# Kernel tuning notes

Hardware: AMD Instinct MI355X
Metric: run time of the kernel (lower is better)

The kernel has to match this reference:

```python
import jax, jax.numpy as jnp
import numpy as np

BN_EPS = 1e-5

def _square_distance(src, dst):
    # src: (B,N,3), dst: (B,S,3) -> (B,N,S)
    d = -2.0 * jnp.einsum('bnc,bsc->bns', src, dst)
    d = d + jnp.sum(src * src, -1)[:, :, None]
    d = d + jnp.sum(dst * dst, -1)[:, None, :]
    return d

def _bn_relu(x, gamma, beta):
    # x: (B,N,C); training-mode batchnorm over (B,N)
    mean = jnp.mean(x, axis=(0, 1))
    var = jnp.mean(jnp.square(x - mean), axis=(0, 1))
    y = (x - mean) * jax.lax.rsqrt(var + BN_EPS) * gamma + beta
    return jax.nn.relu(y)

def setup_inputs() -> dict:
    key = jax.random.key(0)
    ks = jax.random.split(key, 12)
    B, N, S, D1, D2 = 8, 8192, 2048, 128, 256
    in_ch, mlp = 384, [256, 256]
    inp = {
        'xyz1': jax.random.normal(ks[0], (B, 3, N), jnp.float32),
        'xyz2': jax.random.normal(ks[1], (B, 3, S), jnp.float32),
        'points1': jax.random.normal(ks[2], (B, D1, N), jnp.float32),
        'points2': jax.random.normal(ks[3], (B, D2, S), jnp.float32),
    }
    last = in_ch
    for i, out in enumerate(mlp):
        inp[f'W{i+1}'] = jax.random.normal(ks[4 + 2 * i], (out, last), jnp.float32) * (1.0 / np.sqrt(last))
        inp[f'b{i+1}'] = jnp.zeros((out,), jnp.float32)
        inp[f'g{i+1}'] = jnp.ones((out,), jnp.float32)
        inp[f'beta{i+1}'] = jnp.zeros((out,), jnp.float32)
        last = out
    return inp

def reference(xyz1, xyz2, points1, points2, W1, b1, g1, beta1, W2, b2, g2, beta2):
    p1 = jnp.transpose(xyz1, (0, 2, 1))   # (B,N,3)
    p2 = jnp.transpose(xyz2, (0, 2, 1))   # (B,S,3)
    f2 = jnp.transpose(points2, (0, 2, 1))  # (B,S,D2)

    dists = _square_distance(p1, p2)      # (B,N,S)
    neg_d, idx = jax.lax.top_k(-dists, 3)  # 3 smallest distances
    d3 = -neg_d                            # (B,N,3)
    dist_recip = 1.0 / (d3 + 1e-8)
    weight = dist_recip / jnp.sum(dist_recip, axis=2, keepdims=True)  # (B,N,3)

    gathered = jax.vmap(lambda p, i: p[i])(f2, idx)   # (B,N,3,D2)
    interp = jnp.sum(gathered * weight[..., None], axis=2)  # (B,N,D2)

    f1 = jnp.transpose(points1, (0, 2, 1))  # (B,N,D1)
    x = jnp.concatenate([f1, interp], axis=-1)  # (B,N,D1+D2)

    x = _bn_relu(jnp.einsum('bnc,oc->bno', x, W1) + b1, g1, beta1)
    x = _bn_relu(jnp.einsum('bnc,oc->bno', x, W2) + b2, g2, beta2)
    return jnp.transpose(x, (0, 2, 1))  # (B,256,N)
```

## Files before the change

kernel.cpp:

```cpp
#include <hip/hip_runtime.h>

#define B_   8
#define N_   8192
#define S_   2048
#define D1_  128
#define D2_  256
#define O_   256
#define BN_  (B_*N_)

typedef __bf16 bf16;
typedef __bf16 bf16x8_t __attribute__((ext_vector_type(8)));
typedef __bf16 bf16x4_t __attribute__((ext_vector_type(4)));
typedef float  f32x4_t  __attribute__((ext_vector_type(4)));

static const size_t OFF_IDX  = 0;
static const size_t OFF_W    = 786432;
static const size_t OFF_XP   = 1572864;
static const size_t OFF_Z    = 51904512;
static const size_t OFF_SS1  = 85458944;
static const size_t OFF_SS2  = 85460992;
static const size_t OFF_PART = 85463040;

__global__ __launch_bounds__(256) void k_conv_p1(const float* __restrict__ p1, bf16* __restrict__ xp) {
  const int g  = blockIdx.x * 256 + threadIdx.x;
  const int n4 = g & 2047;
  const int c8 = (g >> 11) & 15;
  const int b  = g >> 15;
  const int n  = n4 * 4;
  const float* src = p1 + ((size_t)b * D1_ + c8 * 8) * N_ + n;
  bf16x8_t o0, o1, o2, o3;
  #pragma unroll
  for (int j = 0; j < 8; ++j) {
    float4 v = *(const float4*)(src + (size_t)j * N_);
    o0[j] = (bf16)v.x; o1[j] = (bf16)v.y; o2[j] = (bf16)v.z; o3[j] = (bf16)v.w;
  }
  bf16* dst = xp + (((size_t)b * 48 + c8) * N_ + n) * 8;
  *(bf16x8_t*)(dst)      = o0;
  *(bf16x8_t*)(dst + 8)  = o1;
  *(bf16x8_t*)(dst + 16) = o2;
  *(bf16x8_t*)(dst + 24) = o3;
}

__device__ __forceinline__ void ins3(float d, int i,
                                     float& d0, float& d1, float& d2,
                                     int& i0, int& i1, int& i2) {
  const bool c2 = d < d2, c1 = d < d1, c0 = d < d0;
  const float nd2 = c1 ? d1 : (c2 ? d : d2); const int ni2 = c1 ? i1 : (c2 ? i : i2);
  const float nd1 = c0 ? d0 : (c1 ? d : d1); const int ni1 = c0 ? i0 : (c1 ? i : i1);
  d0 = c0 ? d : d0; i0 = c0 ? i : i0;
  d1 = nd1; i1 = ni1; d2 = nd2; i2 = ni2;
}

__global__ __launch_bounds__(256) void k_nn3(const float* __restrict__ xyz1, const float* __restrict__ xyz2,
                                             int* __restrict__ idxw, float* __restrict__ www) {
  __shared__ float4 sq[4][S_ / 4];
  __shared__ float  pd[4][64][3];
  __shared__ int    pi[4][64][3];
  const int tid  = threadIdx.x;
  const int lane = tid & 63, w = tid >> 6;
  const int b     = blockIdx.y;
  const int nbase = blockIdx.x * 64;

  const float* x2 = xyz2 + (size_t)b * 3 * S_;
  for (int j = tid; j < S_ / 4; j += 256) {
    const float4 x = *(const float4*)(x2 + 4 * j);
    const float4 y = *(const float4*)(x2 + S_ + 4 * j);
    const float4 z = *(const float4*)(x2 + 2 * S_ + 4 * j);
    float4 qq;
    qq.x = fmaf(x.x, x.x, fmaf(y.x, y.x, z.x * z.x));
    qq.y = fmaf(x.y, x.y, fmaf(y.y, y.y, z.y * z.y));
    qq.z = fmaf(x.z, x.z, fmaf(y.z, y.z, z.z * z.z));
    qq.w = fmaf(x.w, x.w, fmaf(y.w, y.w, z.w * z.w));
    sq[0][j] = x; sq[1][j] = y; sq[2][j] = z; sq[3][j] = qq;
  }

  const int n = nbase + lane;
  const float* x1 = xyz1 + (size_t)b * 3 * N_;
  const float px = x1[n], py = x1[N_ + n], pz = x1[2 * N_ + n];
  const float ax = -2.f * px, ay = -2.f * py, az = -2.f * pz;
  __syncthreads();

  float e0 = 3.4e38f, e1 = 3.4e38f, e2 = 3.4e38f;
  int   i0 = 0, i1 = 0, i2 = 0;

  const int jb = w * (S_ / 16);
  #pragma unroll 4
  for (int j = jb; j < jb + S_ / 16; ++j) {
    const float4 qx = sq[0][j], qy = sq[1][j], qz = sq[2][j], qq = sq[3][j];
    #define CAND(C, SI)                                                        \
      {                                                                        \
        const float E = fmaf(ax, qx.C, fmaf(ay, qy.C, fmaf(az, qz.C, qq.C))); \
        const bool l0 = E < e0, l1 = E < e1, l2 = E < e2;                      \
        const int ni1 = l0 ? i0 : (l1 ? (SI) : i1);                            \
        const int ni2 = l1 ? i1 : (l2 ? (SI) : i2);                            \
        i0 = l0 ? (SI) : i0; i1 = ni1; i2 = ni2;                               \
        const float ne1 = __builtin_amdgcn_fmed3f(E, e0, e1);                  \
        const float ne2 = __builtin_amdgcn_fmed3f(E, e1, e2);                  \
        e0 = fminf(E, e0); e1 = ne1; e2 = ne2;                                 \
      }
    CAND(x, 4 * j + 0)
    CAND(y, 4 * j + 1)
    CAND(z, 4 * j + 2)
    CAND(w, 4 * j + 3)
    #undef CAND
  }

  const float pp = fmaf(px, px, fmaf(py, py, pz * pz));
  pd[w][lane][0] = e0 + pp; pd[w][lane][1] = e1 + pp; pd[w][lane][2] = e2 + pp;
  pi[w][lane][0] = i0; pi[w][lane][1] = i1; pi[w][lane][2] = i2;
  __syncthreads();

  if (tid < 64) {
    float d0 = pd[0][tid][0], d1 = pd[0][tid][1], d2 = pd[0][tid][2];
    int   j0 = pi[0][tid][0], j1 = pi[0][tid][1], j2 = pi[0][tid][2];
    #pragma unroll
    for (int ck = 1; ck < 4; ++ck)
      #pragma unroll
      for (int k = 0; k < 3; ++k)
        ins3(pd[ck][tid][k], pi[ck][tid][k], d0, d1, d2, j0, j1, j2);
    const float r0 = 1.f / (d0 + 1e-8f), r1 = 1.f / (d1 + 1e-8f), r2 = 1.f / (d2 + 1e-8f);
    const float inv = 1.f / (r0 + r1 + r2);
    const int bn = b * N_ + nbase + tid;
    idxw[bn] = j0; idxw[BN_ + bn] = j1; idxw[2 * BN_ + bn] = j2;
    www[bn] = r0 * inv; www[BN_ + bn] = r1 * inv; www[2 * BN_ + bn] = r2 * inv;
  }
}

__global__ __launch_bounds__(256) void k_t2(const float* __restrict__ p2, bf16* __restrict__ f2t) {
  __shared__ float lds[64][65];
  const int bid = blockIdx.x;
  const int b = bid & 7;
  const int inner = bid >> 3;
  const int s0 = (inner & 31) * 64;
  const int c0 = (inner >> 5) * 64;
  const int t = threadIdx.x;
  {
    const int cr = t >> 2, scb = (t & 3) * 16;
    const float* src = p2 + ((size_t)b * D2_ + c0 + cr) * S_ + s0 + scb;
    #pragma unroll
    for (int i = 0; i < 4; ++i) {
      const float4 v = *(const float4*)(src + 4 * i);
      lds[cr][scb + 4 * i + 0] = v.x; lds[cr][scb + 4 * i + 1] = v.y;
      lds[cr][scb + 4 * i + 2] = v.z; lds[cr][scb + 4 * i + 3] = v.w;
    }
  }
  __syncthreads();
  const int co = (t & 7) * 8;
  #pragma unroll
  for (int pass = 0; pass < 2; ++pass) {
    const int s = pass * 32 + (t >> 3);
    bf16x8_t o;
    #pragma unroll
    for (int j = 0; j < 8; ++j) o[j] = (bf16)lds[co + j][s];
    *(bf16x8_t*)(f2t + ((size_t)b * S_ + s0 + s) * D2_ + c0 + co) = o;
  }
}

__global__ __launch_bounds__(256) void k_interp(const bf16* __restrict__ f2t, const int* __restrict__ idxw,
                                                const float* __restrict__ www, bf16* __restrict__ xp) {
  const int bid = blockIdx.x;
  const int b = bid & 7;
  const int n = (bid >> 3) * 8 + (threadIdx.x & 7);
  const int c8 = threadIdx.x >> 3;
  const int bn = b * N_ + n;
  const int j0 = idxw[bn], j1 = idxw[BN_ + bn], j2 = idxw[2 * BN_ + bn];
  const float w0 = www[bn], w1 = www[BN_ + bn], w2 = www[2 * BN_ + bn];
  const bf16* base = f2t + (size_t)b * S_ * D2_ + c8 * 8;
  const bf16x8_t v0 = *(const bf16x8_t*)(base + (size_t)j0 * D2_);
  const bf16x8_t v1 = *(const bf16x8_t*)(base + (size_t)j1 * D2_);
  const bf16x8_t v2 = *(const bf16x8_t*)(base + (size_t)j2 * D2_);
  bf16x8_t out;
  #pragma unroll
  for (int j = 0; j < 8; ++j)
    out[j] = (bf16)(w0 * (float)v0[j] + w1 * (float)v1[j] + w2 * (float)v2[j]);
  *(bf16x8_t*)(xp + (((size_t)b * 48 + 16 + c8) * N_ + (size_t)n) * 8) = out;
}

template<int K>
__global__ __launch_bounds__(256) void k_gemm(const float* __restrict__ W, const float* __restrict__ bias,
                                              const bf16* __restrict__ X, bf16* __restrict__ Zp) {
  __shared__ bf16 As[128][40];
  __shared__ bf16 Bt[128][40];
  const int tid = threadIdx.x;
  const int lane = tid & 63, wid = tid >> 6;
  const int wr = wid >> 1, wc = wid & 1;
  const int n0 = blockIdx.x * 128;
  const int m0 = blockIdx.y * 128;
  const int b  = blockIdx.z;
  const int l15 = lane & 15, l4 = lane >> 4;

  f32x4_t acc[4][4];
  #pragma unroll
  for (int i = 0; i < 4; ++i)
    #pragma unroll
    for (int j = 0; j < 4; ++j) { f32x4_t z = {0.f, 0.f, 0.f, 0.f}; acc[i][j] = z; }

  const int arow = tid >> 1, ac0 = (tid & 1) * 16;
  const bf16* Xb = X + (size_t)b * (K / 8) * ((size_t)N_ * 8);

  for (int kt = 0; kt < K; kt += 32) {
    {
      const float* s = W + (size_t)(m0 + arow) * K + kt + ac0;
      const float4 f0 = *(const float4*)(s);
      const float4 f1 = *(const float4*)(s + 4);
      const float4 f2 = *(const float4*)(s + 8);
      const float4 f3 = *(const float4*)(s + 12);
      bf16x8_t h0, h1;
      h0[0] = (bf16)f0.x; h0[1] = (bf16)f0.y; h0[2] = (bf16)f0.z; h0[3] = (bf16)f0.w;
      h0[4] = (bf16)f1.x; h0[5] = (bf16)f1.y; h0[6] = (bf16)f1.z; h0[7] = (bf16)f1.w;
      h1[0] = (bf16)f2.x; h1[1] = (bf16)f2.y; h1[2] = (bf16)f2.z; h1[3] = (bf16)f2.w;
      h1[4] = (bf16)f3.x; h1[5] = (bf16)f3.y; h1[6] = (bf16)f3.z; h1[7] = (bf16)f3.w;
      *(bf16x8_t*)&As[arow][ac0]     = h0;
      *(bf16x8_t*)&As[arow][ac0 + 8] = h1;
    }
    {
      const bf16* s = Xb + ((size_t)(kt / 8 + wid)) * ((size_t)N_ * 8) + (size_t)n0 * 8;
      const bf16x8_t q0 = *(const bf16x8_t*)(s + (size_t)lane * 8);
      const bf16x8_t q1 = *(const bf16x8_t*)(s + (size_t)(lane + 64) * 8);
      *(bf16x8_t*)&Bt[lane][wid * 8]      = q0;
      *(bf16x8_t*)&Bt[lane + 64][wid * 8] = q1;
    }
    __syncthreads();
    bf16x8_t af[4], bfr[4];
    #pragma unroll
    for (int mi = 0; mi < 4; ++mi) af[mi]  = *(const bf16x8_t*)&As[wr * 64 + mi * 16 + l15][l4 * 8];
    #pragma unroll
    for (int ni = 0; ni < 4; ++ni) bfr[ni] = *(const bf16x8_t*)&Bt[wc * 64 + ni * 16 + l15][l4 * 8];
    #pragma unroll
    for (int mi = 0; mi < 4; ++mi)
      #pragma unroll
      for (int ni = 0; ni < 4; ++ni)
        acc[mi][ni] = __builtin_amdgcn_mfma_f32_16x16x32_bf16(af[mi], bfr[ni], acc[mi][ni], 0, 0, 0);
    __syncthreads();
  }
  bf16* Zb = Zp + (size_t)b * 32 * ((size_t)N_ * 8);
  #pragma unroll
  for (int mi = 0; mi < 4; ++mi) {
    const int obase = m0 + wr * 64 + mi * 16 + l4 * 4;
    const float4 bv = *(const float4*)(bias + obase);
    const size_t gofs = (size_t)(obase >> 3) * ((size_t)N_ * 8) + (obase & 7);
    #pragma unroll
    for (int ni = 0; ni < 4; ++ni) {
      const int nn = n0 + wc * 64 + ni * 16 + l15;
      bf16x4_t o;
      o[0] = (bf16)(acc[mi][ni][0] + bv.x);
      o[1] = (bf16)(acc[mi][ni][1] + bv.y);
      o[2] = (bf16)(acc[mi][ni][2] + bv.z);
      o[3] = (bf16)(acc[mi][ni][3] + bv.w);
      *(bf16x4_t*)(Zb + gofs + (size_t)nn * 8) = o;
    }
  }
}

__global__ __launch_bounds__(256) void k_stats_p(const bf16* __restrict__ Z, float* __restrict__ part) {
  const int og = blockIdx.x & 31, b = blockIdx.x >> 5;
  const bf16* src = Z + ((size_t)b * 32 + og) * ((size_t)N_ * 8);
  float s[8], q[8];
  #pragma unroll
  for (int j = 0; j < 8; ++j) { s[j] = 0.f; q[j] = 0.f; }
  for (int n = threadIdx.x; n < N_; n += 256) {
    const bf16x8_t v = *(const bf16x8_t*)(src + (size_t)n * 8);
    #pragma unroll
    for (int j = 0; j < 8; ++j) {
      const float f = (float)v[j];
      s[j] += f; q[j] = fmaf(f, f, q[j]);
    }
  }
  #pragma unroll
  for (int off = 1; off < 64; off <<= 1) {
    #pragma unroll
    for (int j = 0; j < 8; ++j) {
      s[j] += __shfl_xor(s[j], off);
      q[j] += __shfl_xor(q[j], off);
    }
  }
  __shared__ float red[4][16];
  const int w = threadIdx.x >> 6;
  if ((threadIdx.x & 63) == 0) {
    #pragma unroll
    for (int j = 0; j < 8; ++j) { red[w][j] = s[j]; red[w][8 + j] = q[j]; }
  }
  __syncthreads();
  if (threadIdx.x < 16) {
    const float t = red[0][threadIdx.x] + red[1][threadIdx.x] + red[2][threadIdx.x] + red[3][threadIdx.x];
    const int sel = threadIdx.x >> 3, j = threadIdx.x & 7;
    part[((size_t)sel * 256 + og * 8 + j) * 8 + b] = t;
  }
}

__global__ __launch_bounds__(256) void k_ss(const float* __restrict__ part, const float* __restrict__ g,
                                            const float* __restrict__ be, float* __restrict__ ss) {
  const int c = threadIdx.x;
  float s = 0.f, q = 0.f;
  #pragma unroll
  for (int b = 0; b < 8; ++b) { s += part[(size_t)c * 8 + b]; q += part[(256 + (size_t)c) * 8 + b]; }
  const float mean = s * (1.f / 65536.f);
  const float var  = q * (1.f / 65536.f) - mean * mean;
  const float rstd = rsqrtf(var + 1e-5f);
  const float sc = g[c] * rstd;
  ss[c] = sc; ss[O_ + c] = be[c] - mean * sc;
}

__global__ __launch_bounds__(256) void k_apply_p(bf16* __restrict__ Z, const float* __restrict__ ss) {
  const int nc = blockIdx.x & 31, og = (blockIdx.x >> 5) & 31, b = blockIdx.x >> 10;
  const int n = nc * 256 + threadIdx.x;
  bf16* p = Z + (((size_t)b * 32 + og) * N_ + n) * 8;
  bf16x8_t v = *(bf16x8_t*)p;
  #pragma unroll
  for (int j = 0; j < 8; ++j) {
    const int c = og * 8 + j;
    v[j] = (bf16)fmaxf(fmaf((float)v[j], ss[c], ss[O_ + c]), 0.f);
  }
  *(bf16x8_t*)p = v;
}

__global__ __launch_bounds__(256) void k_final_p(const bf16* __restrict__ Z, const float* __restrict__ ss,
                                                 float* __restrict__ Y) {
  const int b  = blockIdx.x >> 7;
  const int n0 = (blockIdx.x & 127) * 64;
  const int og = threadIdx.x >> 3, ns = threadIdx.x & 7;
  const bf16* src = Z + (((size_t)b * 32 + og) * N_ + n0 + ns * 8) * 8;
  bf16x8_t v[8];
  #pragma unroll
  for (int i = 0; i < 8; ++i) v[i] = *(const bf16x8_t*)(src + i * 8);
  float sc[8], sh[8];
  #pragma unroll
  for (int j = 0; j < 8; ++j) { sc[j] = ss[og * 8 + j]; sh[j] = ss[O_ + og * 8 + j]; }
  float* dst = Y + ((size_t)b * O_ + og * 8) * N_ + n0 + ns * 8;
  #pragma unroll
  for (int j = 0; j < 8; ++j) {
    float4 a0, a1;
    a0.x = fmaxf(fmaf((float)v[0][j], sc[j], sh[j]), 0.f);
    a0.y = fmaxf(fmaf((float)v[1][j], sc[j], sh[j]), 0.f);
    a0.z = fmaxf(fmaf((float)v[2][j], sc[j], sh[j]), 0.f);
    a0.w = fmaxf(fmaf((float)v[3][j], sc[j], sh[j]), 0.f);
    a1.x = fmaxf(fmaf((float)v[4][j], sc[j], sh[j]), 0.f);
    a1.y = fmaxf(fmaf((float)v[5][j], sc[j], sh[j]), 0.f);
    a1.z = fmaxf(fmaf((float)v[6][j], sc[j], sh[j]), 0.f);
    a1.w = fmaxf(fmaf((float)v[7][j], sc[j], sh[j]), 0.f);
    *(float4*)(dst + (size_t)j * N_)     = a0;
    *(float4*)(dst + (size_t)j * N_ + 4) = a1;
  }
}

extern "C" void kernel_launch(void* const* d_in, const int* in_sizes, int n_in,
                              void* d_out, int out_size, void* d_ws, size_t ws_size,
                              hipStream_t stream) {
  const float* xyz1    = (const float*)d_in[0];
  const float* xyz2    = (const float*)d_in[1];
  const float* points1 = (const float*)d_in[2];
  const float* points2 = (const float*)d_in[3];
  const float* W1  = (const float*)d_in[4];
  const float* b1  = (const float*)d_in[5];
  const float* g1  = (const float*)d_in[6];
  const float* be1 = (const float*)d_in[7];
  const float* W2  = (const float*)d_in[8];
  const float* b2  = (const float*)d_in[9];
  const float* g2  = (const float*)d_in[10];
  const float* be2 = (const float*)d_in[11];
  float* Y = (float*)d_out;
  char*  ws = (char*)d_ws;
  int*   idxw = (int*)(ws + OFF_IDX);
  float* www  = (float*)(ws + OFF_W);
  bf16*  xp   = (bf16*)(ws + OFF_XP);
  bf16*  z1   = (bf16*)(ws + OFF_Z);
  bf16*  f2t  = (bf16*)(ws + OFF_Z);
  bf16*  z2   = (bf16*)(ws + OFF_XP);
  float* ss1  = (float*)(ws + OFF_SS1);
  float* ss2  = (float*)(ws + OFF_SS2);
  float* part = (float*)(ws + OFF_PART);

  hipLaunchKernelGGL(k_conv_p1, dim3(1024), dim3(256), 0, stream, points1, xp);
  hipLaunchKernelGGL(k_nn3, dim3(128, 8), dim3(256), 0, stream, xyz1, xyz2, idxw, www);
  hipLaunchKernelGGL(k_t2, dim3(1024), dim3(256), 0, stream, points2, f2t);
  hipLaunchKernelGGL(k_interp, dim3(8192), dim3(256), 0, stream, f2t, idxw, www, xp);
  hipLaunchKernelGGL((k_gemm<384>), dim3(64, 2, 8), dim3(256), 0, stream, W1, b1, xp, z1);
  hipLaunchKernelGGL(k_stats_p, dim3(256), dim3(256), 0, stream, z1, part);
  hipLaunchKernelGGL(k_ss, dim3(1), dim3(256), 0, stream, part, g1, be1, ss1);
  hipLaunchKernelGGL(k_apply_p, dim3(8192), dim3(256), 0, stream, z1, ss1);
  hipLaunchKernelGGL((k_gemm<256>), dim3(64, 2, 8), dim3(256), 0, stream, W2, b2, z1, z2);
  hipLaunchKernelGGL(k_stats_p, dim3(256), dim3(256), 0, stream, z2, part);
  hipLaunchKernelGGL(k_ss, dim3(1), dim3(256), 0, stream, part, g2, be2, ss2);
  hipLaunchKernelGGL(k_final_p, dim3(1024), dim3(256), 0, stream, z2, ss2, Y);
}
```

Baseline: 196.4 us.

## Pre-convert weights to bf16 tile images and load GEMM tiles via global_load_lds

Adds a small kernel that converts W1/W2 to bf16 and lays them out in per-tile, k-chunk-major images. The GEMM then fills both shared-memory tiles with direct global-to-LDS 16-byte loads instead of register round-trips and per-iteration fp32-to-bf16 conversion. It also remaps the 1D grid so blocks sharing n-tiles land on the same XCD for L2 reuse. The unpadded LDS layout may raise bank conflicts on fragment reads, and there is one extra launch. The weight images reuse the idx workspace region, which is safe only because the interpolation kernel has already consumed it.

```diff
diff --git a/kernel.cpp b/kernel.cpp
--- a/kernel.cpp
+++ b/kernel.cpp
@@ -20,6 +20,10 @@
 static const size_t OFF_SS1  = 85458944;
 static const size_t OFF_SS2  = 85460992;
 static const size_t OFF_PART = 85463040;
+
+#define GL16(gsrc, ldst) \
+  __builtin_amdgcn_global_load_lds((const __attribute__((address_space(1))) void*)(gsrc), \
+                                   (__attribute__((address_space(3))) void*)(ldst), 16, 0, 0)
 
 __global__ __launch_bounds__(256) void k_conv_p1(const float* __restrict__ p1, bf16* __restrict__ xp) {
   const int g  = blockIdx.x * 256 + threadIdx.x;
@@ -176,17 +180,48 @@
   *(bf16x8_t*)(xp + (((size_t)b * 48 + 16 + c8) * N_ + (size_t)n) * 8) = out;
 }
 
+__global__ __launch_bounds__(256) void k_wprep(const float* __restrict__ W1, const float* __restrict__ W2,
+                                               bf16* __restrict__ img) {
+  const int g = blockIdx.x * 256 + threadIdx.x;
+  if (g < 12288) {
+    const int e = g * 8;
+    const int imgblk = e >> 12, r = e & 4095;
+    const int kc = r >> 10, row = (r & 1023) >> 3;
+    const int mblk = imgblk / 12, kt32 = imgblk % 12;
+    const float* s = W1 + (size_t)(mblk * 128 + row) * 384 + kt32 * 32 + kc * 8;
+    const float4 f0 = *(const float4*)(s), f1 = *(const float4*)(s + 4);
+    bf16x8_t h;
+    h[0] = (bf16)f0.x; h[1] = (bf16)f0.y; h[2] = (bf16)f0.z; h[3] = (bf16)f0.w;
+    h[4] = (bf16)f1.x; h[5] = (bf16)f1.y; h[6] = (bf16)f1.z; h[7] = (bf16)f1.w;
+    *(bf16x8_t*)(img + e) = h;
+  } else if (g < 20480) {
+    const int e = (g - 12288) * 8;
+    const int imgblk = e >> 12, r = e & 4095;
+    const int kc = r >> 10, row = (r & 1023) >> 3;
+    const int mblk = imgblk >> 3, kt32 = imgblk & 7;
+    const float* s = W2 + (size_t)(mblk * 128 + row) * 256 + kt32 * 32 + kc * 8;
+    const float4 f0 = *(const float4*)(s), f1 = *(const float4*)(s + 4);
+    bf16x8_t h;
+    h[0] = (bf16)f0.x; h[1] = (bf16)f0.y; h[2] = (bf16)f0.z; h[3] = (bf16)f0.w;
+    h[4] = (bf16)f1.x; h[5] = (bf16)f1.y; h[6] = (bf16)f1.z; h[7] = (bf16)f1.w;
+    *(bf16x8_t*)(img + 98304 + e) = h;
+  }
+}
+
 template<int K>
-__global__ __launch_bounds__(256) void k_gemm(const float* __restrict__ W, const float* __restrict__ bias,
+__global__ __launch_bounds__(256) void k_gemm(const bf16* __restrict__ Wimg, const float* __restrict__ bias,
                                               const bf16* __restrict__ X, bf16* __restrict__ Zp) {
-  __shared__ bf16 As[128][40];
-  __shared__ bf16 Bt[128][40];
+  __shared__ bf16 As[4096];
+  __shared__ bf16 Bt[4096];
   const int tid = threadIdx.x;
   const int lane = tid & 63, wid = tid >> 6;
   const int wr = wid >> 1, wc = wid & 1;
-  const int n0 = blockIdx.x * 128;
-  const int m0 = blockIdx.y * 128;
-  const int b  = blockIdx.z;
+  const int dd = blockIdx.x;
+  const int xcd = dd & 7, pos = dd >> 3;
+  const int b = pos >> 4, q = pos & 15;
+  const int m0 = (q & 1) * 128;
+  const int n0 = (xcd * 8 + (q >> 1)) * 128;
+  const int mblk = m0 >> 7;
   const int l15 = lane & 15, l4 = lane >> 4;
 
   f32x4_t acc[4][4];
@@ -195,37 +230,21 @@
     #pragma unroll
     for (int j = 0; j < 4; ++j) { f32x4_t z = {0.f, 0.f, 0.f, 0.f}; acc[i][j] = z; }
 
-  const int arow = tid >> 1, ac0 = (tid & 1) * 16;
   const bf16* Xb = X + (size_t)b * (K / 8) * ((size_t)N_ * 8);
 
   for (int kt = 0; kt < K; kt += 32) {
-    {
-      const float* s = W + (size_t)(m0 + arow) * K + kt + ac0;
-      const float4 f0 = *(const float4*)(s);
-      const float4 f1 = *(const float4*)(s + 4);
-      const float4 f2 = *(const float4*)(s + 8);
-      const float4 f3 = *(const float4*)(s + 12);
-      bf16x8_t h0, h1;
-      h0[0] = (bf16)f0.x; h0[1] = (bf16)f0.y; h0[2] = (bf16)f0.z; h0[3] = (bf16)f0.w;
-      h0[4] = (bf16)f1.x; h0[5] = (bf16)f1.y; h0[6] = (bf16)f1.z; h0[7] = (bf16)f1.w;
-      h1[0] = (bf16)f2.x; h1[1] = (bf16)f2.y; h1[2] = (bf16)f2.z; h1[3] = (bf16)f2.w;
-      h1[4] = (bf16)f3.x; h1[5] = (bf16)f3.y; h1[6] = (bf16)f3.z; h1[7] = (bf16)f3.w;
-      *(bf16x8_t*)&As[arow][ac0]     = h0;
-      *(bf16x8_t*)&As[arow][ac0 + 8] = h1;
-    }
-    {
-      const bf16* s = Xb + ((size_t)(kt / 8 + wid)) * ((size_t)N_ * 8) + (size_t)n0 * 8;
-      const bf16x8_t q0 = *(const bf16x8_t*)(s + (size_t)lane * 8);
-      const bf16x8_t q1 = *(const bf16x8_t*)(s + (size_t)(lane + 64) * 8);
-      *(bf16x8_t*)&Bt[lane][wid * 8]      = q0;
-      *(bf16x8_t*)&Bt[lane + 64][wid * 8] = q1;
-    }
+    const bf16* asrc = Wimg + (size_t)(mblk * (K / 32) + (kt >> 5)) * 4096 + wid * 1024 + lane * 8;
+    GL16(asrc,       &As[wid * 1024]);
+    GL16(asrc + 512, &As[wid * 1024 + 512]);
+    const bf16* bsrc = Xb + ((size_t)(kt >> 3) + wid) * ((size_t)N_ * 8) + ((size_t)n0 + lane) * 8;
+    GL16(bsrc,       &Bt[wid * 1024]);
+    GL16(bsrc + 512, &Bt[wid * 1024 + 512]);
     __syncthreads();
     bf16x8_t af[4], bfr[4];
     #pragma unroll
-    for (int mi = 0; mi < 4; ++mi) af[mi]  = *(const bf16x8_t*)&As[wr * 64 + mi * 16 + l15][l4 * 8];
-    #pragma unroll
-    for (int ni = 0; ni < 4; ++ni) bfr[ni] = *(const bf16x8_t*)&Bt[wc * 64 + ni * 16 + l15][l4 * 8];
+    for (int mi = 0; mi < 4; ++mi) af[mi]  = *(const bf16x8_t*)&As[l4 * 1024 + (wr * 64 + mi * 16 + l15) * 8];
+    #pragma unroll
+    for (int ni = 0; ni < 4; ++ni) bfr[ni] = *(const bf16x8_t*)&Bt[l4 * 1024 + (wc * 64 + ni * 16 + l15) * 8];
     #pragma unroll
     for (int mi = 0; mi < 4; ++mi)
       #pragma unroll
@@ -360,25 +379,28 @@
   const float* be2 = (const float*)d_in[11];
   float* Y = (float*)d_out;
   char*  ws = (char*)d_ws;
-  int*   idxw = (int*)(ws + OFF_IDX);
-  float* www  = (float*)(ws + OFF_W);
-  bf16*  xp   = (bf16*)(ws + OFF_XP);
-  bf16*  z1   = (bf16*)(ws + OFF_Z);
-  bf16*  f2t  = (bf16*)(ws + OFF_Z);
-  bf16*  z2   = (bf16*)(ws + OFF_XP);
-  float* ss1  = (float*)(ws + OFF_SS1);
-  float* ss2  = (float*)(ws + OFF_SS2);
-  float* part = (float*)(ws + OFF_PART);
+  int*   idxw  = (int*)(ws + OFF_IDX);
+  float* www   = (float*)(ws + OFF_W);
+  bf16*  wimg1 = (bf16*)(ws + OFF_IDX);
+  bf16*  wimg2 = wimg1 + 98304;
+  bf16*  xp    = (bf16*)(ws + OFF_XP);
+  bf16*  z1    = (bf16*)(ws + OFF_Z);
+  bf16*  f2t   = (bf16*)(ws + OFF_Z);
+  bf16*  z2    = (bf16*)(ws + OFF_XP);
+  float* ss1   = (float*)(ws + OFF_SS1);
+  float* ss2   = (float*)(ws + OFF_SS2);
+  float* part  = (float*)(ws + OFF_PART);
 
   hipLaunchKernelGGL(k_conv_p1, dim3(1024), dim3(256), 0, stream, points1, xp);
   hipLaunchKernelGGL(k_nn3, dim3(128, 8), dim3(256), 0, stream, xyz1, xyz2, idxw, www);
   hipLaunchKernelGGL(k_t2, dim3(1024), dim3(256), 0, stream, points2, f2t);
   hipLaunchKernelGGL(k_interp, dim3(8192), dim3(256), 0, stream, f2t, idxw, www, xp);
-  hipLaunchKernelGGL((k_gemm<384>), dim3(64, 2, 8), dim3(256), 0, stream, W1, b1, xp, z1);
+  hipLaunchKernelGGL(k_wprep, dim3(80), dim3(256), 0, stream, W1, W2, wimg1);
+  hipLaunchKernelGGL((k_gemm<384>), dim3(1024), dim3(256), 0, stream, wimg1, b1, xp, z1);
   hipLaunchKernelGGL(k_stats_p, dim3(256), dim3(256), 0, stream, z1, part);
   hipLaunchKernelGGL(k_ss, dim3(1), dim3(256), 0, stream, part, g1, be1, ss1);
   hipLaunchKernelGGL(k_apply_p, dim3(8192), dim3(256), 0, stream, z1, ss1);
-  hipLaunchKernelGGL((k_gemm<256>), dim3(64, 2, 8), dim3(256), 0, stream, W2, b2, z1, z2);
+  hipLaunchKernelGGL((k_gemm<256>), dim3(1024), dim3(256), 0, stream, wimg2, b2, z1, z2);
   hipLaunchKernelGGL(k_stats_p, dim3(256), dim3(256), 0, stream, z2, part);
   hipLaunchKernelGGL(k_ss, dim3(1), dim3(256), 0, stream, part, g2, be2, ss2);
   hipLaunchKernelGGL(k_final_p, dim3(1024), dim3(256), 0, stream, z2, ss2, Y);
```

Result: faster. 190.8 us (-2.8%).
